# Kernel tuning notes

Measured on AMD Instinct MI355X. Metric: run time of the kernel, lower is better.

Reference implementation:

```python
import jax, jax.numpy as jnp
import numpy as np

CAR_DIM = 8
ESC_MAX_AGENT = 32
HID = 256
ACTION_DIM = 30
NUM_STATES = 64
BATCH = 8192
ENC_OUT = 1 + CAR_DIM * ESC_MAX_AGENT          # 257
Q_IN = 1 + CAR_DIM + CAR_DIM * ESC_MAX_AGENT   # 265


def setup_inputs() -> dict:
    key = jax.random.key(0)
    ks = jax.random.split(key, 9)
    s = jax.random.normal(ks[0], (BATCH, CAR_DIM + NUM_STATES * CAR_DIM), dtype=jnp.float32)
    def lin(k, fan_in, fan_out):
        bound = 1.0 / np.sqrt(fan_in)
        kw, kb = jax.random.split(k)
        W = jax.random.uniform(kw, (fan_in, fan_out), jnp.float32, -bound, bound)
        b = jax.random.uniform(kb, (fan_out,), jnp.float32, -bound, bound)
        return W, b
    W1, b1 = lin(ks[1], CAR_DIM, HID)
    W2, b2 = lin(ks[2], HID, ENC_OUT)
    Qw1, Qb1 = lin(ks[3], Q_IN, HID)
    Qw2, Qb2 = lin(ks[4], HID, ACTION_DIM)
    return {"s": s, "W1": W1, "b1": b1, "W2": W2, "b2": b2,
            "Qw1": Qw1, "Qb1": Qb1, "Qw2": Qw2, "Qb2": Qb2}


def reference(s, W1, b1, W2, b2, Qw1, Qb1, Qw2, Qb2):
    B = s.shape[0]
    self_states = s[:, :CAR_DIM]                                   # [B, C]
    surr = s[:, CAR_DIM:].reshape(B, -1, CAR_DIM)                  # [B, N, C]
    # sentinel agents: any coordinate exactly == -1 is skipped
    valid = ~jnp.any(surr == -1.0, axis=-1)                        # [B, N] bool
    h = jax.nn.relu(jnp.einsum('bnc,ch->bnh', surr, W1) + b1)      # [B, N, HID]
    enc = jax.nn.relu(jnp.einsum('bnh,he->bne', h, W2) + b2)       # [B, N, ENC_OUT]
    sum_outputs = jnp.sum(enc * valid[:, :, None].astype(enc.dtype), axis=1)  # [B, ENC_OUT]
    x = jnp.concatenate([self_states, sum_outputs], axis=1)        # [B, Q_IN]
    q = jax.nn.relu(x @ Qw1 + Qb1) @ Qw2 + Qb2                     # [B, ACTION_DIM]
    return q
```

## Files before the change

### kernel.cpp

```cpp
#include <hip/hip_runtime.h>

#define CAR 8
#define SROW 520
#define HID 256
#define EOUT 257
#define XPAD 288
#define ADIM 30

typedef __attribute__((ext_vector_type(8))) short sh8;
typedef __attribute__((ext_vector_type(4))) float f32x4;

__device__ __forceinline__ short f2bf(float f) {
  unsigned u = __builtin_bit_cast(unsigned, f);
  u += 0x7fffu + ((u >> 16) & 1u);
  return (short)(u >> 16);
}
__device__ __forceinline__ unsigned f2bf2(float a, float b) {
  unsigned ua = __builtin_bit_cast(unsigned, a);
  ua += 0x7fffu + ((ua >> 16) & 1u);
  unsigned ub = __builtin_bit_cast(unsigned, b);
  ub += 0x7fffu + ((ub >> 16) & 1u);
  return __builtin_amdgcn_perm(ub, ua, 0x07060302);
}
__device__ __forceinline__ unsigned pkt(float a, float b) {
  return __builtin_amdgcn_perm(__builtin_bit_cast(unsigned, b),
                               __builtin_bit_cast(unsigned, a), 0x07060302);
}

__global__ void k_prep(const float* __restrict__ W1, const float* __restrict__ b1,
                       const float* __restrict__ W2,
                       const float* __restrict__ Qw1, const float* __restrict__ Qw2,
                       short* __restrict__ w1f, short* __restrict__ w2f,
                       short* __restrict__ w3f, short* __restrict__ wq2f) {
  int idx = blockIdx.x * 256 + threadIdx.x;
  if (idx < 8192) {
    int mt = idx >> 9, r = idx & 511, lane = r >> 3, j = r & 7;
    int quad = lane >> 4, m = lane & 15;
    int hid = mt * 16 + m;
    float v = (quad == 0) ? W1[j * HID + hid]
            : (quad == 1 && j == 0) ? b1[hid] : 0.0f;
    w1f[idx] = f2bf(v);
    return;
  }
  int i2 = idx - 8192;
  if (i2 < 69632) {
    int ks = i2 / 8704, r = i2 % 8704;
    int nt = r >> 9, r2 = r & 511, lane = r2 >> 3, j = r2 & 7;
    int quad = lane >> 4, m = lane & 15;
    int k = ks * 32 + quad * 8 + j, n = nt * 16 + m;
    float v = (n < EOUT) ? W2[k * EOUT + n] : 0.0f;
    w2f[i2] = f2bf(v);
    return;
  }
  int i3 = i2 - 69632;
  if (i3 < 73728) {
    int ks = i3 >> 13, r = i3 & 8191;
    int nt = r >> 9, r2 = r & 511, lane = r2 >> 3, j = r2 & 7;
    int quad = lane >> 4, m = lane & 15;
    int k = ks * 32 + quad * 8 + j, n = nt * 16 + m;
    float v = (k < 265) ? Qw1[k * HID + n] : 0.0f;
    w3f[i3] = f2bf(v);
    return;
  }
  int i4 = i3 - 73728;
  if (i4 < 8192) {
    int ks = i4 >> 10, r = i4 & 1023;
    int nt = r >> 9, r2 = r & 511, lane = r2 >> 3, j = r2 & 7;
    int quad = lane >> 4, m = lane & 15;
    int k = ks * 32 + quad * 8 + j, n = nt * 16 + m;
    float v = (n < ADIM) ? Qw2[k * ADIM + n] : 0.0f;
    wq2f[i4] = f2bf(v);
  }
}

__global__ __launch_bounds__(256, 3)
void k_enc(const float* __restrict__ s, const short* __restrict__ w1f,
           const short* __restrict__ w2f, const float* __restrict__ b2,
           short* __restrict__ sob, int B) {
  __shared__ __align__(16) short hlds[16384];
  __shared__ float psum[256];
  __shared__ float ninvp[4];

  const int tid = threadIdx.x;
  const int w = tid >> 6, lane = tid & 63;
  const int q = lane >> 4, m = lane & 15;
  const int b = blockIdx.x;
  const float* srow0 = s + (size_t)b * SROW + CAR;

  int dA = 0, dB = 0, invAi = 0;
  if (lane < 32) {
    const float* sr = srow0 + (16 * w + (lane >> 1)) * CAR + (lane & 1) * 4;
    float4 f = *(const float4*)sr;
    int inv4 = (f.x == -1.f) | (f.y == -1.f) | (f.z == -1.f) | (f.w == -1.f);
    invAi = inv4 | __shfl_xor(inv4, 1, 64);
    if (!invAi) { dA = (int)f2bf2(f.x, f.y); dB = (int)f2bf2(f.z, f.w); }
  }
  {
    unsigned long long bal = __ballot((lane < 32) && !(lane & 1) && invAi);
    if (lane == 0) ninvp[w] = (float)__popcll(bal);
  }
  const int src = 2 * m;
  int g0 = __shfl(dA, src, 64), g1 = __shfl(dB, src, 64);
  int g2 = __shfl(dA, src + 1, 64), g3 = __shfl(dB, src + 1, 64);
  int invm = __shfl(invAi, src, 64);
  int4 bv;
  if (q == 0)      bv = (int4){g0, g1, g2, g3};
  else if (q == 1) bv = (int4){invm ? 0 : 0x3f80, 0, 0, 0};
  else             bv = (int4){0, 0, 0, 0};
  sh8 bs = __builtin_bit_cast(sh8, bv);

#pragma unroll
  for (int mt = 0; mt < 16; ++mt) {
    sh8 af = *(const sh8*)(w1f + (mt * 64 + lane) * 8);
    f32x4 z = {0.f, 0.f, 0.f, 0.f};
    f32x4 c = __builtin_amdgcn_mfma_f32_16x16x32_bf16(af, bs, z, 0, 0, 0);
    const int hidb = mt * 16 + q * 4;
    const int ks = hidb >> 5, qB = (hidb >> 3) & 3, js = hidb & 7;
    uint2 k0;
    k0.x = pkt(fmaxf(c[0], 0.f), fmaxf(c[1], 0.f));
    k0.y = pkt(fmaxf(c[2], 0.f), fmaxf(c[3], 0.f));
    *(uint2*)(&hlds[((w * 8 + ks) * 64 + qB * 16 + m) * 8 + js]) = k0;
  }
  __syncthreads();

  f32x4 acc[4][4];
  f32x4 acc16[4];
#pragma unroll
  for (int Mt = 0; Mt < 4; ++Mt) {
#pragma unroll
    for (int i = 0; i < 4; ++i) {
      f32x4 z = {0.f, 0.f, 0.f, 0.f};
      acc[Mt][i] = z;
    }
    f32x4 z = {0.f, 0.f, 0.f, 0.f};
    acc16[Mt] = z;
  }

#pragma unroll
  for (int ks = 0; ks < 8; ++ks) {
    sh8 A[4];
#pragma unroll
    for (int Mt = 0; Mt < 4; ++Mt)
      A[Mt] = *(const sh8*)(&hlds[((Mt * 8 + ks) * 64 + lane) * 8]);
    sh8 Bf[4];
#pragma unroll
    for (int i = 0; i < 4; ++i)
      Bf[i] = *(const sh8*)(w2f + ((ks * 17 + 4 * w + i) * 64 + lane) * 8);
#pragma unroll
    for (int i = 0; i < 4; ++i)
#pragma unroll
      for (int Mt = 0; Mt < 4; ++Mt)
        acc[Mt][i] = __builtin_amdgcn_mfma_f32_16x16x32_bf16(A[Mt], Bf[i], acc[Mt][i], 0, 0, 0);
    if ((ks >> 1) == w) {
      sh8 Bt = *(const sh8*)(w2f + ((ks * 17 + 16) * 64 + lane) * 8);
#pragma unroll
      for (int Mt = 0; Mt < 4; ++Mt)
        acc16[Mt] = __builtin_amdgcn_mfma_f32_16x16x32_bf16(A[Mt], Bt, acc16[Mt], 0, 0, 0);
    }
  }

  const float ninv = ninvp[0] + ninvp[1] + ninvp[2] + ninvp[3];
#pragma unroll
  for (int i = 0; i < 4; ++i) {
    const int col = (4 * w + i) * 16 + m;
    const float b2c = b2[col];
    float ssum = 0.f;
#pragma unroll
    for (int Mt = 0; Mt < 4; ++Mt)
#pragma unroll
      for (int r = 0; r < 4; ++r)
        ssum += fmaxf(acc[Mt][i][r] + b2c, 0.f);
    ssum += __shfl_xor(ssum, 16, 64);
    ssum += __shfl_xor(ssum, 32, 64);
    ssum -= ninv * fmaxf(b2c, 0.f);
    if (q == 0)
      sob[(size_t)b * XPAD + CAR + col] = f2bf(ssum);
  }
  if (m == 0) {
#pragma unroll
    for (int Mt = 0; Mt < 4; ++Mt)
#pragma unroll
      for (int r = 0; r < 4; ++r)
        psum[w * 64 + Mt * 16 + q * 4 + r] = acc16[Mt][r];
  }
  __syncthreads();

  if (w == 0) {
    float tot = psum[lane] + psum[64 + lane] + psum[128 + lane] + psum[192 + lane];
    const float b2c = b2[256];
    float v = fmaxf(tot + b2c, 0.f);
#pragma unroll
    for (int msk = 1; msk < 64; msk <<= 1)
      v += __shfl_xor(v, msk, 64);
    if (lane == 0)
      sob[(size_t)b * XPAD + CAR + 256] = f2bf(v - ninv * fmaxf(b2c, 0.f));
  }
  if (w == 1 && lane < CAR)
    sob[(size_t)b * XPAD + lane] = f2bf(s[(size_t)b * SROW + lane]);
}

__global__ __launch_bounds__(256, 2)
void k_q(const short* __restrict__ sob, const short* __restrict__ w3f,
         const float* __restrict__ Qb1, const short* __restrict__ wq2f,
         const float* __restrict__ Qb2, float* __restrict__ out, int B) {
  __shared__ __align__(16) float H[32 * 260];
  const int tid = threadIdx.x;
  const int w = tid >> 6, lane = tid & 63;
  const int q = lane >> 4, m = lane & 15;
  const int b0 = blockIdx.x * 32;
  int r0 = b0 + m;      if (r0 >= B) r0 = B - 1;
  int r1 = b0 + 16 + m; if (r1 >= B) r1 = B - 1;
  const short* xr0 = sob + (size_t)r0 * XPAD + q * 8;
  const short* xr1 = sob + (size_t)r1 * XPAD + q * 8;

  f32x4 acc1[2][4];
#pragma unroll
  for (int mt = 0; mt < 2; ++mt)
#pragma unroll
    for (int i = 0; i < 4; ++i) {
      f32x4 z = {0.f, 0.f, 0.f, 0.f};
      acc1[mt][i] = z;
    }
#pragma unroll
  for (int ks = 0; ks < 9; ++ks) {
    sh8 A0 = *(const sh8*)(xr0 + ks * 32);
    sh8 A1 = *(const sh8*)(xr1 + ks * 32);
#pragma unroll
    for (int i = 0; i < 4; ++i) {
      sh8 Bf = *(const sh8*)(w3f + ((ks * 16 + 4 * w + i) * 64 + lane) * 8);
      acc1[0][i] = __builtin_amdgcn_mfma_f32_16x16x32_bf16(A0, Bf, acc1[0][i], 0, 0, 0);
      acc1[1][i] = __builtin_amdgcn_mfma_f32_16x16x32_bf16(A1, Bf, acc1[1][i], 0, 0, 0);
    }
  }
#pragma unroll
  for (int i = 0; i < 4; ++i) {
    const int hcol = (4 * w + i) * 16 + m;
    const float bq = Qb1[hcol];
#pragma unroll
    for (int mt = 0; mt < 2; ++mt)
#pragma unroll
      for (int r = 0; r < 4; ++r)
        H[(mt * 16 + q * 4 + r) * 260 + hcol] = fmaxf(acc1[mt][i][r] + bq, 0.f);
  }
  __syncthreads();

  const int mt2 = w >> 1, nt2 = w & 1;
  f32x4 acc2 = {0.f, 0.f, 0.f, 0.f};
#pragma unroll
  for (int ks = 0; ks < 8; ++ks) {
    const float* hp = H + (mt2 * 16 + m) * 260 + ks * 32 + q * 8;
    float4 ha = ((const float4*)hp)[0], hb = ((const float4*)hp)[1];
    int4 t = {(int)f2bf2(ha.x, ha.y), (int)f2bf2(ha.z, ha.w),
              (int)f2bf2(hb.x, hb.y), (int)f2bf2(hb.z, hb.w)};
    sh8 A2 = __builtin_bit_cast(sh8, t);
    sh8 Bf = *(const sh8*)(wq2f + ((ks * 2 + nt2) * 64 + lane) * 8);
    acc2 = __builtin_amdgcn_mfma_f32_16x16x32_bf16(A2, Bf, acc2, 0, 0, 0);
  }
  const int act = nt2 * 16 + m;
  if (act < ADIM) {
    const float bq = Qb2[act];
#pragma unroll
    for (int r = 0; r < 4; ++r) {
      const int row = b0 + mt2 * 16 + q * 4 + r;
      if (row < B) out[(size_t)row * ADIM + act] = acc2[r] + bq;
    }
  }
}

extern "C" void kernel_launch(void* const* d_in, const int* in_sizes, int n_in,
                              void* d_out, int out_size, void* d_ws, size_t ws_size,
                              hipStream_t stream) {
  const float* s   = (const float*)d_in[0];
  const float* W1  = (const float*)d_in[1];
  const float* b1  = (const float*)d_in[2];
  const float* W2  = (const float*)d_in[3];
  const float* b2  = (const float*)d_in[4];
  const float* Qw1 = (const float*)d_in[5];
  const float* Qb1 = (const float*)d_in[6];
  const float* Qw2 = (const float*)d_in[7];
  const float* Qb2 = (const float*)d_in[8];
  float* out = (float*)d_out;
  const int B = in_sizes[0] / SROW;

  char* wsb = (char*)d_ws;
  short* sob = (short*)wsb;
  size_t off = (size_t)B * XPAD * sizeof(short);
  short* w1f  = (short*)(wsb + off);            off += 8192 * 2;
  short* w2f  = (short*)(wsb + off);            off += 69632 * 2;
  short* w3f  = (short*)(wsb + off);            off += 73728 * 2;
  short* wq2f = (short*)(wsb + off);

  const int prep_elems = 8192 + 69632 + 73728 + 8192;
  k_prep<<<(prep_elems + 255) / 256, 256, 0, stream>>>(W1, b1, W2, Qw1, Qw2,
                                                       w1f, w2f, w3f, wq2f);
  k_enc<<<B, 256, 0, stream>>>(s, w1f, w2f, b2, sob, B);
  k_q<<<(B + 31) / 32, 256, 0, stream>>>(sob, w3f, Qb1, wq2f, Qb2, out, B);
}
```

Before: 165.1 us.

## Fold layer-2 bias into GEMM as extra K-slice and software-pipeline operand loads

Appends b2 as a 257th K row in the packed W2 fragments and adds a ninth K-step, where the hidden activations carry a validity flag (1 for valid agents, 0 for sentinel ones). Masking and bias then both come out of the MFMA. This removes the per-column b2 loads, the ballot/popcount invalid-count correction, and its shared memory. The W2 fragment layout is regrouped by N-tile so each wave walks a contiguous stream, and the next K-step's A/B fragments are prefetched into registers to overlap loads with MFMAs. The cost is one extra MFMA K-step, higher register pressure from double buffering, and bf16 rounding of the bias.

```diff
diff --git a/kernel.cpp b/kernel.cpp
--- a/kernel.cpp
+++ b/kernel.cpp
@@ -28,7 +28,7 @@
 }
 
 __global__ void k_prep(const float* __restrict__ W1, const float* __restrict__ b1,
-                       const float* __restrict__ W2,
+                       const float* __restrict__ W2, const float* __restrict__ b2,
                        const float* __restrict__ Qw1, const float* __restrict__ Qw2,
                        short* __restrict__ w1f, short* __restrict__ w2f,
                        short* __restrict__ w3f, short* __restrict__ wq2f) {
@@ -43,16 +43,20 @@
     return;
   }
   int i2 = idx - 8192;
-  if (i2 < 69632) {
-    int ks = i2 / 8704, r = i2 % 8704;
-    int nt = r >> 9, r2 = r & 511, lane = r2 >> 3, j = r2 & 7;
+  if (i2 < 78336) {
+    int nt = i2 / 4608, r = i2 % 4608;
+    int ks = r >> 9, r2 = r & 511, lane = r2 >> 3, j = r2 & 7;
     int quad = lane >> 4, m = lane & 15;
     int k = ks * 32 + quad * 8 + j, n = nt * 16 + m;
-    float v = (n < EOUT) ? W2[k * EOUT + n] : 0.0f;
+    float v = 0.0f;
+    if (n < EOUT) {
+      if (k < 256)       v = W2[k * EOUT + n];
+      else if (k == 256) v = b2[n];
+    }
     w2f[i2] = f2bf(v);
     return;
   }
-  int i3 = i2 - 69632;
+  int i3 = i2 - 78336;
   if (i3 < 73728) {
     int ks = i3 >> 13, r = i3 & 8191;
     int nt = r >> 9, r2 = r & 511, lane = r2 >> 3, j = r2 & 7;
@@ -75,11 +79,9 @@
 
 __global__ __launch_bounds__(256, 3)
 void k_enc(const float* __restrict__ s, const short* __restrict__ w1f,
-           const short* __restrict__ w2f, const float* __restrict__ b2,
-           short* __restrict__ sob, int B) {
-  __shared__ __align__(16) short hlds[16384];
-  __shared__ float psum[256];
-  __shared__ float ninvp[4];
+           const short* __restrict__ w2f, short* __restrict__ sob, int B) {
+  __shared__ __align__(16) short hlds[4 * 9 * 512];
+  __shared__ float psum[4][64];
 
   const int tid = threadIdx.x;
   const int w = tid >> 6, lane = tid & 63;
@@ -95,19 +97,21 @@
     invAi = inv4 | __shfl_xor(inv4, 1, 64);
     if (!invAi) { dA = (int)f2bf2(f.x, f.y); dB = (int)f2bf2(f.z, f.w); }
   }
-  {
-    unsigned long long bal = __ballot((lane < 32) && !(lane & 1) && invAi);
-    if (lane == 0) ninvp[w] = (float)__popcll(bal);
-  }
   const int src = 2 * m;
   int g0 = __shfl(dA, src, 64), g1 = __shfl(dB, src, 64);
   int g2 = __shfl(dA, src + 1, 64), g3 = __shfl(dB, src + 1, 64);
   int invm = __shfl(invAi, src, 64);
+  const int flagbits = invm ? 0 : 0x3f80;
   int4 bv;
   if (q == 0)      bv = (int4){g0, g1, g2, g3};
-  else if (q == 1) bv = (int4){invm ? 0 : 0x3f80, 0, 0, 0};
+  else if (q == 1) bv = (int4){flagbits, 0, 0, 0};
   else             bv = (int4){0, 0, 0, 0};
   sh8 bs = __builtin_bit_cast(sh8, bv);
+
+  {
+    int4 v4 = {(q == 0) ? flagbits : 0, 0, 0, 0};
+    *(int4*)(&hlds[((w * 9 + 8) * 64 + lane) * 8]) = v4;
+  }
 
 #pragma unroll
   for (int mt = 0; mt < 16; ++mt) {
@@ -119,7 +123,7 @@
     uint2 k0;
     k0.x = pkt(fmaxf(c[0], 0.f), fmaxf(c[1], 0.f));
     k0.y = pkt(fmaxf(c[2], 0.f), fmaxf(c[3], 0.f));
-    *(uint2*)(&hlds[((w * 8 + ks) * 64 + qB * 16 + m) * 8 + js]) = k0;
+    *(uint2*)(&hlds[((w * 9 + ks) * 64 + qB * 16 + m) * 8 + js]) = k0;
   }
   __syncthreads();
 
@@ -136,43 +140,56 @@
     acc16[Mt] = z;
   }
 
-#pragma unroll
-  for (int ks = 0; ks < 8; ++ks) {
-    sh8 A[4];
-#pragma unroll
-    for (int Mt = 0; Mt < 4; ++Mt)
-      A[Mt] = *(const sh8*)(&hlds[((Mt * 8 + ks) * 64 + lane) * 8]);
-    sh8 Bf[4];
-#pragma unroll
-    for (int i = 0; i < 4; ++i)
-      Bf[i] = *(const sh8*)(w2f + ((ks * 17 + 4 * w + i) * 64 + lane) * 8);
+  const short* w2b = w2f + (size_t)(4 * w) * 9 * 512 + lane * 8;
+  const short* hb  = hlds + lane * 8;
+
+  sh8 A[4], Bf[4];
+#pragma unroll
+  for (int Mt = 0; Mt < 4; ++Mt) A[Mt] = *(const sh8*)(hb + Mt * 9 * 512);
+#pragma unroll
+  for (int i = 0; i < 4; ++i)    Bf[i] = *(const sh8*)(w2b + i * 9 * 512);
+
+#pragma unroll
+  for (int ks = 0; ks < 9; ++ks) {
+    sh8 An[4], Bn[4];
+    if (ks < 8) {
+#pragma unroll
+      for (int Mt = 0; Mt < 4; ++Mt)
+        An[Mt] = *(const sh8*)(hb + (Mt * 9 + ks + 1) * 512);
+#pragma unroll
+      for (int i = 0; i < 4; ++i)
+        Bn[i] = *(const sh8*)(w2b + (i * 9 + ks + 1) * 512);
+    }
 #pragma unroll
     for (int i = 0; i < 4; ++i)
 #pragma unroll
       for (int Mt = 0; Mt < 4; ++Mt)
         acc[Mt][i] = __builtin_amdgcn_mfma_f32_16x16x32_bf16(A[Mt], Bf[i], acc[Mt][i], 0, 0, 0);
-    if ((ks >> 1) == w) {
-      sh8 Bt = *(const sh8*)(w2f + ((ks * 17 + 16) * 64 + lane) * 8);
+    if (ks == w || ks == w + 4 || (ks == 8 && w == 0)) {
+      sh8 Bt = *(const sh8*)(w2f + (size_t)(16 * 9 + ks) * 512 + lane * 8);
 #pragma unroll
       for (int Mt = 0; Mt < 4; ++Mt)
         acc16[Mt] = __builtin_amdgcn_mfma_f32_16x16x32_bf16(A[Mt], Bt, acc16[Mt], 0, 0, 0);
     }
-  }
-
-  const float ninv = ninvp[0] + ninvp[1] + ninvp[2] + ninvp[3];
+    if (ks < 8) {
+#pragma unroll
+      for (int Mt = 0; Mt < 4; ++Mt) A[Mt] = An[Mt];
+#pragma unroll
+      for (int i = 0; i < 4; ++i)    Bf[i] = Bn[i];
+    }
+  }
+
 #pragma unroll
   for (int i = 0; i < 4; ++i) {
     const int col = (4 * w + i) * 16 + m;
-    const float b2c = b2[col];
     float ssum = 0.f;
 #pragma unroll
     for (int Mt = 0; Mt < 4; ++Mt)
 #pragma unroll
       for (int r = 0; r < 4; ++r)
-        ssum += fmaxf(acc[Mt][i][r] + b2c, 0.f);
+        ssum += fmaxf(acc[Mt][i][r], 0.f);
     ssum += __shfl_xor(ssum, 16, 64);
     ssum += __shfl_xor(ssum, 32, 64);
-    ssum -= ninv * fmaxf(b2c, 0.f);
     if (q == 0)
       sob[(size_t)b * XPAD + CAR + col] = f2bf(ssum);
   }
@@ -181,19 +198,18 @@
     for (int Mt = 0; Mt < 4; ++Mt)
 #pragma unroll
       for (int r = 0; r < 4; ++r)
-        psum[w * 64 + Mt * 16 + q * 4 + r] = acc16[Mt][r];
+        psum[w][Mt * 16 + q * 4 + r] = acc16[Mt][r];
   }
   __syncthreads();
 
   if (w == 0) {
-    float tot = psum[lane] + psum[64 + lane] + psum[128 + lane] + psum[192 + lane];
-    const float b2c = b2[256];
-    float v = fmaxf(tot + b2c, 0.f);
+    float tot = psum[0][lane] + psum[1][lane] + psum[2][lane] + psum[3][lane];
+    float v = fmaxf(tot, 0.f);
 #pragma unroll
     for (int msk = 1; msk < 64; msk <<= 1)
       v += __shfl_xor(v, msk, 64);
     if (lane == 0)
-      sob[(size_t)b * XPAD + CAR + 256] = f2bf(v - ninv * fmaxf(b2c, 0.f));
+      sob[(size_t)b * XPAD + CAR + 256] = f2bf(v);
   }
   if (w == 1 && lane < CAR)
     sob[(size_t)b * XPAD + lane] = f2bf(s[(size_t)b * SROW + lane]);
@@ -286,13 +302,13 @@
   short* sob = (short*)wsb;
   size_t off = (size_t)B * XPAD * sizeof(short);
   short* w1f  = (short*)(wsb + off);            off += 8192 * 2;
-  short* w2f  = (short*)(wsb + off);            off += 69632 * 2;
+  short* w2f  = (short*)(wsb + off);            off += 78336 * 2;
   short* w3f  = (short*)(wsb + off);            off += 73728 * 2;
   short* wq2f = (short*)(wsb + off);
 
-  const int prep_elems = 8192 + 69632 + 73728 + 8192;
-  k_prep<<<(prep_elems + 255) / 256, 256, 0, stream>>>(W1, b1, W2, Qw1, Qw2,
+  const int prep_elems = 8192 + 78336 + 73728 + 8192;
+  k_prep<<<(prep_elems + 255) / 256, 256, 0, stream>>>(W1, b1, W2, b2, Qw1, Qw2,
                                                        w1f, w2f, w3f, wq2f);
-  k_enc<<<B, 256, 0, stream>>>(s, w1f, w2f, b2, sob, B);
+  k_enc<<<B, 256, 0, stream>>>(s, w1f, w2f, sob, B);
   k_q<<<(B + 31) / 32, 256, 0, stream>>>(sob, w3f, Qb1, wq2f, Qb2, out, B);
 }
```

Measured after the change: 164.6 us. Within noise of the previous version (-0.3%).
